# Performance work log

Hardware: AMD Instinct MI355X
Metric: run time of the kernel (lower is better)

## Reference

```python
import jax, jax.numpy as jnp
import numpy as np

B, T, IN, OUT, R = 4096, 8, 1024, 1024, 32

def setup_inputs() -> dict:
    key = jax.random.key(0)
    k1, k2, k3, k4 = jax.random.split(key, 4)
    return {
        "x": jax.random.normal(k1, (B, T, IN), dtype=jnp.float32),
        "first_shared_core": jax.random.normal(k2, (T, R), dtype=jnp.float32) * 0.1,
        "middle_shared_core": jax.random.normal(k3, (R, IN, R), dtype=jnp.float32) * 0.1,
        "task_core": jax.random.normal(k4, (R, OUT), dtype=jnp.float32) * 0.1,
    }

def reference(x, first_shared_core, middle_shared_core, task_core):
    # contract TT cores -> per-task weight [T, IN, OUT]
    w = jnp.einsum('tj,jik->tik', first_shared_core, middle_shared_core)
    w = jnp.einsum('tik,ko->tio', w, task_core)
    # per-task batched matmul: [B,T,IN] x [T,IN,OUT] -> [B,T,OUT]
    return jnp.einsum('bti,tio->bto', x, w)
```

## Files before the change

### kernel.cpp

```cpp
#include <hip/hip_runtime.h>
#include <hip/hip_bf16.h>
#include <stdint.h>

#define B_DIM 4096
#define T_DIM 8
#define IN_DIM 1024
#define OUT_DIM 1024
#define R_DIM 32

#define BM 256
#define BN 256
#define BK 64
#define NKT (IN_DIM / BK)

typedef __bf16 bf16x8 __attribute__((ext_vector_type(8)));
typedef float  f32x4  __attribute__((ext_vector_type(4)));

#define VMCNT(n) asm volatile("s_waitcnt vmcnt(" #n ")" ::: "memory")
#define CFENCE() asm volatile("" ::: "memory")
#define BARRIER() do { CFENCE(); __builtin_amdgcn_s_barrier(); CFENCE(); } while (0)


__device__ __forceinline__ uint32_t pack2_bf16(float a, float b) {
  uint32_t ua = __float_as_uint(a), ub = __float_as_uint(b);
  ua = (ua + 0x7FFFu + ((ua >> 16) & 1u)) >> 16;
  ub = (ub + 0x7FFFu + ((ub >> 16) & 1u)) & 0xFFFF0000u;
  return ua | ub;
}

__device__ __forceinline__ void gload_lds16(const void* g, void* l) {
  __builtin_amdgcn_global_load_lds(
      (const __attribute__((address_space(1))) void*)(uintptr_t)g,
      (__attribute__((address_space(3))) void*)(uint32_t)(uintptr_t)l,
      16, 0, 0);
}

__device__ __forceinline__ void stage_half(const uint16_t* gtile, int ktn,
                                           int half, uint8_t* ldsop,
                                           int wave, int lane) {
#pragma unroll
  for (int j = 0; j < 2; ++j) {
    int s = j * 64 + wave * 8 + (lane >> 3);
    int c = lane & 7;
    int row = (s >> 4) * 32 + half * 16 + (s & 15);
    gload_lds16((const uint8_t*)(gtile + (size_t)row * IN_DIM + ktn * BK) +
                    ((c ^ (s & 7)) << 4),
                ldsop + half * 16384 + j * 8192 + wave * 1024);
  }
}

__device__ __forceinline__ bf16x8 lds_frag(const uint8_t* op, int grp,
                                           int par, int ks,
                                           int l15, int kg, int l7) {
  return *(const bf16x8*)(op + par * 16384 + (grp >> 1) * 2048 + l15 * 128 +
                          ((((ks << 2) + kg) ^ l7) << 4));
}

__device__ __forceinline__ void cvt32(const float* src, uint16_t* dst) {
  float4 v[8];
#pragma unroll
  for (int i = 0; i < 8; ++i) v[i] = *(const float4*)(src + i * 4);
#pragma unroll
  for (int i = 0; i < 4; ++i) {
    uint4 o;
    o.x = pack2_bf16(v[2 * i].x, v[2 * i].y);
    o.y = pack2_bf16(v[2 * i].z, v[2 * i].w);
    o.z = pack2_bf16(v[2 * i + 1].x, v[2 * i + 1].y);
    o.w = pack2_bf16(v[2 * i + 1].z, v[2 * i + 1].w);
    *(uint4*)(dst + i * 8) = o;
  }
}

__global__ __launch_bounds__(256) void pre1(const float* __restrict__ first,
                                            const float* __restrict__ middle,
                                            float* __restrict__ a1,
                                            const float* __restrict__ x,
                                            uint16_t* __restrict__ xb) {
  int bid = blockIdx.x, tid = threadIdx.x;
  if (bid < 1024) {
    int idx = bid * 256 + tid;
    int t  = idx >> 15;
    int ik = idx & 32767;
    float acc = 0.f;
#pragma unroll
    for (int j = 0; j < R_DIM; ++j)
      acc = fmaf(first[t * R_DIM + j], middle[j * (IN_DIM * R_DIM) + ik], acc);
    a1[idx] = acc;
  } else {
    int cb = bid - 1024;
    int row_in = tid >> 5;
    int c0 = (tid & 31) * 32;
    int R = cb * 8 + row_in;
    int b = R >> 2, t = R & 3;
    cvt32(x + ((size_t)b * T_DIM + t) * IN_DIM + c0,
          xb + ((size_t)t * B_DIM + b) * IN_DIM + c0);
  }
}

__global__ __launch_bounds__(256) void pre2(const float* __restrict__ a1,
                                            const float* __restrict__ task,
                                            __hip_bfloat16* __restrict__ wT,
                                            const float* __restrict__ x,
                                            uint16_t* __restrict__ xb) {
  int bid = blockIdx.x;
  int tid = threadIdx.x;
  if (bid < 2048) {
    int t  = bid >> 8;
    int ob = (bid >> 4) & 15;
    int ib = bid & 15;
    __shared__ float A1s[64][33];
    __shared__ float Ts[32][64];
#pragma unroll
    for (int r = 0; r < 8; ++r) {
      int idx2 = tid + 256 * r;
      int il = idx2 >> 5, k = idx2 & 31;
      A1s[il][k] = a1[t * (IN_DIM * R_DIM) + (ib * 64 + il) * R_DIM + k];
    }
#pragma unroll
    for (int r = 0; r < 8; ++r) {
      int idx2 = tid + 256 * r;
      int k = idx2 >> 6, ol = idx2 & 63;
      Ts[k][ol] = task[k * OUT_DIM + ob * 64 + ol];
    }
    __syncthreads();
    int il = tid & 63;
    int og = tid >> 6;
    float acc[16];
#pragma unroll
    for (int r = 0; r < 16; ++r) acc[r] = 0.f;
#pragma unroll
    for (int k = 0; k < 32; ++k) {
      float a = A1s[il][k];
#pragma unroll
      for (int r = 0; r < 16; ++r)
        acc[r] = fmaf(a, Ts[k][og * 16 + r], acc[r]);
    }
#pragma unroll
    for (int r = 0; r < 16; ++r) {
      size_t o = (size_t)ob * 64 + og * 16 + r;
      wT[((size_t)t * OUT_DIM + o) * IN_DIM + ib * 64 + il] = __float2bfloat16(acc[r]);
    }
  } else {
    int cb = bid - 2048;
    int row_in = tid >> 5;
    int c0 = (tid & 31) * 32;
    int R = cb * 8 + row_in;
    int b = R >> 2, t = 4 + (R & 3);
    cvt32(x + ((size_t)b * T_DIM + t) * IN_DIM + c0,
          xb + ((size_t)t * B_DIM + b) * IN_DIM + c0);
  }
}

__global__ __launch_bounds__(512, 2) void tt_gemm(const uint16_t* __restrict__ XB,
                                                  const uint16_t* __restrict__ WT,
                                                  float* __restrict__ O) {
  extern __shared__ uint8_t sm[];
  int bid = blockIdx.x;
  const int t  = bid & 7;
  const int l  = bid >> 3;
  const int mt = l >> 2;
  const int nt = l & 3;

  const int tid  = threadIdx.x;
  const int lane = tid & 63;
  const int wave = tid >> 6;
  const int wr = wave >> 2, wc = wave & 3;
  const int wr8 = wr * 8, wc4 = wc * 4;
  const int l15 = lane & 15, l7 = lane & 7, kg = lane >> 4;

  const uint16_t* gA = XB + ((size_t)t * B_DIM + mt * BM) * IN_DIM;
  const uint16_t* gB = WT + ((size_t)t * OUT_DIM + nt * BN) * IN_DIM;

  uint8_t* bA = sm;
  uint8_t* bB = sm + 32768;

  f32x4 acc[8][4] = {};
  bf16x8 afr[4][2], bfr0[2][2], bfr1[2][2];

  stage_half(gA, 0, 0, bA, wave, lane);
  stage_half(gB, 0, 0, bB, wave, lane);
  stage_half(gA, 0, 1, bA, wave, lane);
  stage_half(gB, 0, 1, bB, wave, lane);
  VMCNT(4);
  BARRIER();

  for (int kt = 0; kt < NKT; ++kt) {
    const bool st = (kt + 1) < NKT;

#pragma unroll
    for (int mo = 0; mo < 4; ++mo)
#pragma unroll
      for (int ks = 0; ks < 2; ++ks)
        afr[mo][ks] = lds_frag(bA, wr8 + mo * 2, 0, ks, l15, kg, l7);
#pragma unroll
    for (int no = 0; no < 2; ++no)
#pragma unroll
      for (int ks = 0; ks < 2; ++ks)
        bfr0[no][ks] = lds_frag(bB, wc4 + no * 2, 0, ks, l15, kg, l7);
    VMCNT(0);
    BARRIER();
    __builtin_amdgcn_s_setprio(1);
#pragma unroll
    for (int mo = 0; mo < 4; ++mo)
#pragma unroll
      for (int no = 0; no < 2; ++no)
#pragma unroll
        for (int ks = 0; ks < 2; ++ks)
          acc[mo * 2][no * 2] = __builtin_amdgcn_mfma_f32_16x16x32_bf16(
              afr[mo][ks], bfr0[no][ks], acc[mo * 2][no * 2], 0, 0, 0);
    __builtin_amdgcn_s_setprio(0);
    BARRIER();

#pragma unroll
    for (int no = 0; no < 2; ++no)
#pragma unroll
      for (int ks = 0; ks < 2; ++ks)
        bfr1[no][ks] = lds_frag(bB, wc4 + no * 2 + 1, 1, ks, l15, kg, l7);
    if (st) {
      stage_half(gA, kt + 1, 0, bA, wave, lane);
      stage_half(gB, kt + 1, 0, bB, wave, lane);
    }
    BARRIER();
    __builtin_amdgcn_s_setprio(1);
#pragma unroll
    for (int mo = 0; mo < 4; ++mo)
#pragma unroll
      for (int no = 0; no < 2; ++no)
#pragma unroll
        for (int ks = 0; ks < 2; ++ks)
          acc[mo * 2][no * 2 + 1] = __builtin_amdgcn_mfma_f32_16x16x32_bf16(
              afr[mo][ks], bfr1[no][ks], acc[mo * 2][no * 2 + 1], 0, 0, 0);
    __builtin_amdgcn_s_setprio(0);
    BARRIER();

#pragma unroll
    for (int mo = 0; mo < 4; ++mo)
#pragma unroll
      for (int ks = 0; ks < 2; ++ks)
        afr[mo][ks] = lds_frag(bA, wr8 + mo * 2 + 1, 1, ks, l15, kg, l7);
    BARRIER();
    __builtin_amdgcn_s_setprio(1);
#pragma unroll
    for (int mo = 0; mo < 4; ++mo)
#pragma unroll
      for (int no = 0; no < 2; ++no)
#pragma unroll
        for (int ks = 0; ks < 2; ++ks)
          acc[mo * 2 + 1][no * 2] = __builtin_amdgcn_mfma_f32_16x16x32_bf16(
              afr[mo][ks], bfr0[no][ks], acc[mo * 2 + 1][no * 2], 0, 0, 0);
    __builtin_amdgcn_s_setprio(0);
    BARRIER();

    if (st) {
      stage_half(gA, kt + 1, 1, bA, wave, lane);
      stage_half(gB, kt + 1, 1, bB, wave, lane);
      VMCNT(4);
    }
    BARRIER();
    __builtin_amdgcn_s_setprio(1);
#pragma unroll
    for (int mo = 0; mo < 4; ++mo)
#pragma unroll
      for (int no = 0; no < 2; ++no)
#pragma unroll
        for (int ks = 0; ks < 2; ++ks)
          acc[mo * 2 + 1][no * 2 + 1] = __builtin_amdgcn_mfma_f32_16x16x32_bf16(
              afr[mo][ks], bfr1[no][ks], acc[mo * 2 + 1][no * 2 + 1], 0, 0, 0);
    __builtin_amdgcn_s_setprio(0);
    BARRIER();
  }

  const int crow0 = mt * BM + wr * 128 + (lane >> 4) * 4;
  const int ccol0 = nt * BN + wc * 64 + (lane & 15);
#pragma unroll
  for (int m = 0; m < 8; ++m) {
#pragma unroll
    for (int j = 0; j < 4; ++j) {
      size_t rowoff =
          ((size_t)(crow0 + m * 16 + j) * T_DIM + t) * OUT_DIM + ccol0;
#pragma unroll
      for (int n = 0; n < 4; ++n)
        O[rowoff + n * 16] = acc[m][n][j];
    }
  }
}

extern "C" void kernel_launch(void* const* d_in, const int* in_sizes, int n_in,
                              void* d_out, int out_size, void* d_ws, size_t ws_size,
                              hipStream_t stream) {
  const float* x      = (const float*)d_in[0];
  const float* first  = (const float*)d_in[1];
  const float* middle = (const float*)d_in[2];
  const float* task   = (const float*)d_in[3];
  float* out = (float*)d_out;

  float* a1 = (float*)d_ws;
  __hip_bfloat16* wT = (__hip_bfloat16*)((uint8_t*)d_ws + (1u << 20));
  uint16_t* xb = (uint16_t*)((uint8_t*)d_ws + (17u << 20));

  hipFuncSetAttribute((const void*)tt_gemm,
                      hipFuncAttributeMaxDynamicSharedMemorySize, 65536);

  pre1<<<3072, 256, 0, stream>>>(first, middle, a1, x, xb);
  pre2<<<4096, 256, 0, stream>>>(a1, task, wT, x, xb);
  tt_gemm<<<T_DIM * (B_DIM / BM) * (OUT_DIM / BN), 512, 65536, stream>>>(
      xb, (const uint16_t*)wT, out);
}
```

Before: 152.4 us.

## Fuse x fp32-to-bf16 conversion into GEMM main loop prefetch

Removes the separate x conversion passes from the two precompute kernels. The GEMM kernel now loads its own fp32 rows of x two K-tiles ahead, packs them to bf16 and writes them to the global staging buffer, which is then staged into LDS. The aim is to hide the conversion traffic behind MFMA work and save a full extra pass over x. The cost is that the four column-tile blocks sharing a row tile each read and convert the same x rows redundantly. Correctness also depends on each block's global writes becoming visible to its own global-to-LDS loads through the vmcnt waits and barriers.

```diff
diff --git a/kernel.cpp b/kernel.cpp
--- a/kernel.cpp
+++ b/kernel.cpp
@@ -56,102 +56,63 @@
                           ((((ks << 2) + kg) ^ l7) << 4));
 }
 
-__device__ __forceinline__ void cvt32(const float* src, uint16_t* dst) {
-  float4 v[8];
-#pragma unroll
-  for (int i = 0; i < 8; ++i) v[i] = *(const float4*)(src + i * 4);
-#pragma unroll
-  for (int i = 0; i < 4; ++i) {
-    uint4 o;
-    o.x = pack2_bf16(v[2 * i].x, v[2 * i].y);
-    o.y = pack2_bf16(v[2 * i].z, v[2 * i].w);
-    o.z = pack2_bf16(v[2 * i + 1].x, v[2 * i + 1].y);
-    o.w = pack2_bf16(v[2 * i + 1].z, v[2 * i + 1].w);
-    *(uint4*)(dst + i * 8) = o;
-  }
-}
-
-__global__ __launch_bounds__(256) void pre1(const float* __restrict__ first,
-                                            const float* __restrict__ middle,
-                                            float* __restrict__ a1,
-                                            const float* __restrict__ x,
-                                            uint16_t* __restrict__ xb) {
-  int bid = blockIdx.x, tid = threadIdx.x;
-  if (bid < 1024) {
-    int idx = bid * 256 + tid;
-    int t  = idx >> 15;
-    int ik = idx & 32767;
-    float acc = 0.f;
-#pragma unroll
-    for (int j = 0; j < R_DIM; ++j)
-      acc = fmaf(first[t * R_DIM + j], middle[j * (IN_DIM * R_DIM) + ik], acc);
-    a1[idx] = acc;
-  } else {
-    int cb = bid - 1024;
-    int row_in = tid >> 5;
-    int c0 = (tid & 31) * 32;
-    int R = cb * 8 + row_in;
-    int b = R >> 2, t = R & 3;
-    cvt32(x + ((size_t)b * T_DIM + t) * IN_DIM + c0,
-          xb + ((size_t)t * B_DIM + b) * IN_DIM + c0);
-  }
-}
-
-__global__ __launch_bounds__(256) void pre2(const float* __restrict__ a1,
-                                            const float* __restrict__ task,
-                                            __hip_bfloat16* __restrict__ wT,
-                                            const float* __restrict__ x,
-                                            uint16_t* __restrict__ xb) {
+__global__ void tt_stage1(const float* __restrict__ first,
+                          const float* __restrict__ middle,
+                          float* __restrict__ a1) {
+  int idx = blockIdx.x * 256 + threadIdx.x;
+  int t  = idx >> 15;
+  int ik = idx & 32767;
+  float acc = 0.f;
+#pragma unroll
+  for (int j = 0; j < R_DIM; ++j)
+    acc = fmaf(first[t * R_DIM + j], middle[j * (IN_DIM * R_DIM) + ik], acc);
+  a1[idx] = acc;
+}
+
+__global__ __launch_bounds__(256) void tt_stage2(const float* __restrict__ a1,
+                                                 const float* __restrict__ task,
+                                                 __hip_bfloat16* __restrict__ wT) {
   int bid = blockIdx.x;
+  int t  = bid >> 8;
+  int ob = (bid >> 4) & 15;
+  int ib = bid & 15;
+  __shared__ float A1s[64][33];
+  __shared__ float Ts[32][64];
   int tid = threadIdx.x;
-  if (bid < 2048) {
-    int t  = bid >> 8;
-    int ob = (bid >> 4) & 15;
-    int ib = bid & 15;
-    __shared__ float A1s[64][33];
-    __shared__ float Ts[32][64];
-#pragma unroll
-    for (int r = 0; r < 8; ++r) {
-      int idx2 = tid + 256 * r;
-      int il = idx2 >> 5, k = idx2 & 31;
-      A1s[il][k] = a1[t * (IN_DIM * R_DIM) + (ib * 64 + il) * R_DIM + k];
-    }
-#pragma unroll
-    for (int r = 0; r < 8; ++r) {
-      int idx2 = tid + 256 * r;
-      int k = idx2 >> 6, ol = idx2 & 63;
-      Ts[k][ol] = task[k * OUT_DIM + ob * 64 + ol];
-    }
-    __syncthreads();
-    int il = tid & 63;
-    int og = tid >> 6;
-    float acc[16];
-#pragma unroll
-    for (int r = 0; r < 16; ++r) acc[r] = 0.f;
-#pragma unroll
-    for (int k = 0; k < 32; ++k) {
-      float a = A1s[il][k];
-#pragma unroll
-      for (int r = 0; r < 16; ++r)
-        acc[r] = fmaf(a, Ts[k][og * 16 + r], acc[r]);
-    }
-#pragma unroll
-    for (int r = 0; r < 16; ++r) {
-      size_t o = (size_t)ob * 64 + og * 16 + r;
-      wT[((size_t)t * OUT_DIM + o) * IN_DIM + ib * 64 + il] = __float2bfloat16(acc[r]);
-    }
-  } else {
-    int cb = bid - 2048;
-    int row_in = tid >> 5;
-    int c0 = (tid & 31) * 32;
-    int R = cb * 8 + row_in;
-    int b = R >> 2, t = 4 + (R & 3);
-    cvt32(x + ((size_t)b * T_DIM + t) * IN_DIM + c0,
-          xb + ((size_t)t * B_DIM + b) * IN_DIM + c0);
-  }
-}
-
-__global__ __launch_bounds__(512, 2) void tt_gemm(const uint16_t* __restrict__ XB,
+#pragma unroll
+  for (int r = 0; r < 8; ++r) {
+    int idx2 = tid + 256 * r;
+    int il = idx2 >> 5, k = idx2 & 31;
+    A1s[il][k] = a1[t * (IN_DIM * R_DIM) + (ib * 64 + il) * R_DIM + k];
+  }
+#pragma unroll
+  for (int r = 0; r < 8; ++r) {
+    int idx2 = tid + 256 * r;
+    int k = idx2 >> 6, ol = idx2 & 63;
+    Ts[k][ol] = task[k * OUT_DIM + ob * 64 + ol];
+  }
+  __syncthreads();
+  int il = tid & 63;
+  int og = tid >> 6;
+  float acc[16];
+#pragma unroll
+  for (int r = 0; r < 16; ++r) acc[r] = 0.f;
+#pragma unroll
+  for (int k = 0; k < 32; ++k) {
+    float a = A1s[il][k];
+#pragma unroll
+    for (int r = 0; r < 16; ++r)
+      acc[r] = fmaf(a, Ts[k][og * 16 + r], acc[r]);
+  }
+#pragma unroll
+  for (int r = 0; r < 16; ++r) {
+    size_t o = (size_t)ob * 64 + og * 16 + r;
+    wT[((size_t)t * OUT_DIM + o) * IN_DIM + ib * 64 + il] = __float2bfloat16(acc[r]);
+  }
+}
+
+__global__ __launch_bounds__(512, 2) void tt_gemm(const float* __restrict__ X,
+                                                  uint16_t* __restrict__ XB,
                                                   const uint16_t* __restrict__ WT,
                                                   float* __restrict__ O) {
   extern __shared__ uint8_t sm[];
@@ -168,6 +129,13 @@
   const int wr8 = wr * 8, wc4 = wc * 4;
   const int l15 = lane & 15, l7 = lane & 7, kg = lane >> 4;
 
+  const int row_in = tid >> 1;
+  const int kh = tid & 1;
+  const float* xsrc0 =
+      X + ((size_t)(mt * BM + row_in) * T_DIM + t) * IN_DIM + kh * 32;
+  uint16_t* xdst0 =
+      XB + ((size_t)t * B_DIM + mt * BM + row_in) * IN_DIM + kh * 32;
+
   const uint16_t* gA = XB + ((size_t)t * B_DIM + mt * BM) * IN_DIM;
   const uint16_t* gB = WT + ((size_t)t * OUT_DIM + nt * BN) * IN_DIM;
 
@@ -176,7 +144,26 @@
 
   f32x4 acc[8][4] = {};
   bf16x8 afr[4][2], bfr0[2][2], bfr1[2][2];
-
+  float4 xl[8];
+
+#pragma unroll
+  for (int p = 0; p < 2; ++p) {
+#pragma unroll
+    for (int j = 0; j < 8; ++j)
+      xl[j] = *(const float4*)(xsrc0 + p * BK + j * 4);
+    VMCNT(0);
+#pragma unroll
+    for (int j = 0; j < 4; ++j) {
+      uint4 o;
+      o.x = pack2_bf16(xl[2 * j].x, xl[2 * j].y);
+      o.y = pack2_bf16(xl[2 * j].z, xl[2 * j].w);
+      o.z = pack2_bf16(xl[2 * j + 1].x, xl[2 * j + 1].y);
+      o.w = pack2_bf16(xl[2 * j + 1].z, xl[2 * j + 1].w);
+      *(uint4*)(xdst0 + p * BK + j * 8) = o;
+    }
+  }
+  VMCNT(0);
+  BARRIER();
   stage_half(gA, 0, 0, bA, wave, lane);
   stage_half(gB, 0, 0, bB, wave, lane);
   stage_half(gA, 0, 1, bA, wave, lane);
@@ -186,6 +173,7 @@
 
   for (int kt = 0; kt < NKT; ++kt) {
     const bool st = (kt + 1) < NKT;
+    const bool cv = (kt + 2) < NKT;
 
 #pragma unroll
     for (int mo = 0; mo < 4; ++mo)
@@ -216,6 +204,12 @@
 #pragma unroll
       for (int ks = 0; ks < 2; ++ks)
         bfr1[no][ks] = lds_frag(bB, wc4 + no * 2 + 1, 1, ks, l15, kg, l7);
+    if (cv) {
+      const float* xs = xsrc0 + (size_t)(kt + 2) * BK;
+#pragma unroll
+      for (int j = 0; j < 8; ++j)
+        xl[j] = *(const float4*)(xs + j * 4);
+    }
     if (st) {
       stage_half(gA, kt + 1, 0, bA, wave, lane);
       stage_half(gB, kt + 1, 0, bB, wave, lane);
@@ -238,6 +232,19 @@
 #pragma unroll
       for (int ks = 0; ks < 2; ++ks)
         afr[mo][ks] = lds_frag(bA, wr8 + mo * 2 + 1, 1, ks, l15, kg, l7);
+    if (cv) {
+      VMCNT(4);
+      uint16_t* xd = xdst0 + (size_t)(kt + 2) * BK;
+#pragma unroll
+      for (int j = 0; j < 4; ++j) {
+        uint4 o;
+        o.x = pack2_bf16(xl[2 * j].x, xl[2 * j].y);
+        o.y = pack2_bf16(xl[2 * j].z, xl[2 * j].w);
+        o.z = pack2_bf16(xl[2 * j + 1].x, xl[2 * j + 1].y);
+        o.w = pack2_bf16(xl[2 * j + 1].z, xl[2 * j + 1].w);
+        *(uint4*)(xd + j * 8) = o;
+      }
+    }
     BARRIER();
     __builtin_amdgcn_s_setprio(1);
 #pragma unroll
@@ -254,6 +261,10 @@
     if (st) {
       stage_half(gA, kt + 1, 1, bA, wave, lane);
       stage_half(gB, kt + 1, 1, bB, wave, lane);
+    }
+    if (cv) {
+      VMCNT(8);
+    } else if (st) {
       VMCNT(4);
     }
     BARRIER();
@@ -301,8 +312,8 @@
   hipFuncSetAttribute((const void*)tt_gemm,
                       hipFuncAttributeMaxDynamicSharedMemorySize, 65536);
 
-  pre1<<<3072, 256, 0, stream>>>(first, middle, a1, x, xb);
-  pre2<<<4096, 256, 0, stream>>>(a1, task, wT, x, xb);
+  tt_stage1<<<(T_DIM * IN_DIM * R_DIM) / 256, 256, 0, stream>>>(first, middle, a1);
+  tt_stage2<<<T_DIM * 16 * 16, 256, 0, stream>>>(a1, task, wT);
   tt_gemm<<<T_DIM * (B_DIM / BM) * (OUT_DIM / BN), 512, 65536, stream>>>(
-      xb, (const uint16_t*)wT, out);
-}
+      x, xb, (const uint16_t*)wT, out);
+}
```

New measurement: 261.2 us (median of 2 runs). +71.4%, slower.
